# Kernel optimization log

Measured on AMD Instinct MI355X. Metric: run time of the kernel, lower is better.

## Reference

```python
import jax, jax.numpy as jnp
import numpy as np

B, T, C, H, HS = 4, 2048, 1024, 16, 64
EPS = 1e-5


def setup_inputs() -> dict:
    key = jax.random.key(0)
    ks = jax.random.split(key, 16)
    s = lambda k, shp, fan: jax.random.normal(k, shp, jnp.float32) * (fan ** -0.5)
    return {
        "x": jax.random.normal(ks[0], (B, T, C), jnp.float32),
        "wq": s(ks[1], (H, C, HS), C), "bq": jnp.zeros((H, HS), jnp.float32),
        "wk": s(ks[2], (H, C, HS), C), "bk": jnp.zeros((H, HS), jnp.float32),
        "wv": s(ks[3], (H, C, HS), C), "bv": jnp.zeros((H, HS), jnp.float32),
        "wp": s(ks[4], (C, C), C), "bp": jnp.zeros((C,), jnp.float32),
        "w1": s(ks[5], (C, 4 * C), C), "b1": jnp.zeros((4 * C,), jnp.float32),
        "w2": s(ks[6], (4 * C, C), 4 * C), "b2": jnp.zeros((C,), jnp.float32),
        "g1": jnp.ones((C,), jnp.float32), "be1": jnp.zeros((C,), jnp.float32),
        "g2": jnp.ones((C,), jnp.float32), "be2": jnp.zeros((C,), jnp.float32),
    }


def _layernorm(x, g, b):
    mu = jnp.mean(x, axis=-1, keepdims=True)
    var = jnp.mean(jnp.square(x - mu), axis=-1, keepdims=True)
    return (x - mu) * jax.lax.rsqrt(var + EPS) * g + b


def reference(x, wq, bq, wk, bk, wv, bv, wp, bp, w1, b1, w2, b2, g1, be1, g2, be2):
    Bc, Tc, Cc = x.shape
    h = _layernorm(x, g1, be1)
    # per-head projections stacked: [B,H,T,HS]
    q = jnp.einsum('btc,hcd->bhtd', h, wq) + bq[None, :, None, :]
    k = jnp.einsum('btc,hcd->bhtd', h, wk) + bk[None, :, None, :]
    v = jnp.einsum('btc,hcd->bhtd', h, wv) + bv[None, :, None, :]
    # NOTE: source scales by 1/sqrt(n_embd), not 1/sqrt(head_size)
    scores = jnp.einsum('bhtd,bhsd->bhts', q, k) * (Cc ** -0.5)
    causal = jnp.tril(jnp.ones((Tc, Tc), bool))
    scores = jnp.where(causal, scores, -jnp.inf)
    attn = jax.nn.softmax(scores, axis=-1)
    out = jnp.einsum('bhts,bhsd->bhtd', attn, v)
    out = out.transpose(0, 2, 1, 3).reshape(Bc, Tc, Cc)  # concat heads
    x = x + out @ wp + bp
    h2 = _layernorm(x, g2, be2)
    ffn = jax.nn.relu(h2 @ w1 + b1) @ w2 + b2
    return x + ffn
```

## Files before the change

### kernel.cpp

```cpp
#include <hip/hip_runtime.h>


constexpr int Bb = 4, Tt = 2048, Cc = 1024, Hh = 16, HSz = 64, Ff = 4096;
constexpr int Mrows = Bb * Tt;

typedef __attribute__((ext_vector_type(8))) short bf16x8;
typedef __attribute__((ext_vector_type(4))) float f32x4;

__device__ __forceinline__ ushort f2bf(float f) {
  uint u = __builtin_bit_cast(uint, f);
  uint r = (u + 0x7fffu + ((u >> 16) & 1u)) >> 16;
  return (ushort)r;
}
__device__ __forceinline__ float bf2f(ushort s) {
  return __builtin_bit_cast(float, ((uint)s) << 16);
}
__device__ __forceinline__ uint cvtpk_bf16(float lo, float hi) {
  uint r;
  asm("v_cvt_pk_bf16_f32 %0, %1, %2" : "=v"(r) : "v"(lo), "v"(hi));
  return r;
}
__device__ __forceinline__ void gload16(const void* g, void* l) {
  __builtin_amdgcn_global_load_lds(
      (const __attribute__((address_space(1))) void*)g,
      (__attribute__((address_space(3))) void*)l, 16, 0, 0);
}
#define VMCNT0 asm volatile("s_waitcnt vmcnt(0)" ::: "memory")
#define LGKM0                                          \
  do {                                                 \
    asm volatile("s_waitcnt lgkmcnt(0)" ::: "memory"); \
    __builtin_amdgcn_sched_barrier(0);                 \
  } while (0)
#define BARRIER __builtin_amdgcn_s_barrier()

__global__ __launch_bounds__(256) void ln_kernel(const float* __restrict__ x,
                                                 const float* __restrict__ g,
                                                 const float* __restrict__ b,
                                                 ushort* __restrict__ out) {
  int row = blockIdx.x;
  const float* xr = x + (size_t)row * Cc;
  int c4 = threadIdx.x * 4;
  float4 v = *(const float4*)(xr + c4);
  float s1 = v.x + v.y + v.z + v.w;
  float s2 = v.x * v.x + v.y * v.y + v.z * v.z + v.w * v.w;
#pragma unroll
  for (int off = 32; off >= 1; off >>= 1) {
    s1 += __shfl_xor(s1, off);
    s2 += __shfl_xor(s2, off);
  }
  __shared__ float red[8];
  int wid = threadIdx.x >> 6, lane = threadIdx.x & 63;
  if (lane == 0) { red[wid] = s1; red[4 + wid] = s2; }
  __syncthreads();
  float t1 = red[0] + red[1] + red[2] + red[3];
  float t2 = red[4] + red[5] + red[6] + red[7];
  float mu = t1 * (1.0f / Cc);
  float var = t2 * (1.0f / Cc) - mu * mu;
  float rs = rsqrtf(var + 1e-5f);
  float4 gv = *(const float4*)(g + c4);
  float4 bv = *(const float4*)(b + c4);
  ushort4 o;
  o.x = f2bf((v.x - mu) * rs * gv.x + bv.x);
  o.y = f2bf((v.y - mu) * rs * gv.y + bv.y);
  o.z = f2bf((v.z - mu) * rs * gv.z + bv.z);
  o.w = f2bf((v.w - mu) * rs * gv.w + bv.w);
  *(ushort4*)(out + (size_t)row * Cc + c4) = o;
}

__device__ __forceinline__ void tcast_body(const float* __restrict__ src,
                                           ushort* __restrict__ dst, int ldS,
                                           int ldD, int r0, int c0) {
  __shared__ float t[32][33];
  int c = threadIdx.x & 31, r8 = threadIdx.x >> 5;
#pragma unroll
  for (int i = 0; i < 4; ++i) {
    int r = r8 + i * 8;
    t[r][c] = src[(size_t)(r0 + r) * ldS + c0 + c];
  }
  __syncthreads();
#pragma unroll
  for (int i = 0; i < 4; ++i) {
    int rr = r8 + i * 8;
    dst[(size_t)(c0 + rr) * ldD + r0 + c] = f2bf(t[c][rr]);
  }
}

__global__ __launch_bounds__(256) void tcast_kernel(const float* __restrict__ src,
                                                    ushort* __restrict__ dst,
                                                    int ldS, int ldD) {
  tcast_body(src, dst, ldS, ldD, blockIdx.x * 32, blockIdx.y * 32);
}

__global__ __launch_bounds__(256) void tcast_qkv(const float* __restrict__ wq,
                                                 const float* __restrict__ wk,
                                                 const float* __restrict__ wv,
                                                 ushort* __restrict__ dst) {
  int z = blockIdx.z, zz = z >> 4, h = z & 15;
  const float* src = (zz == 0 ? wq : (zz == 1 ? wk : wv)) + (size_t)h * Cc * HSz;
  ushort* d = dst + (size_t)(zz * 1024 + h * 64) * 1024;
  tcast_body(src, d, HSz, Cc, blockIdx.x * 32, blockIdx.y * 32);
}

__global__ __launch_bounds__(256) void bias_concat(const float* __restrict__ bq,
                                                   const float* __restrict__ bk,
                                                   const float* __restrict__ bv,
                                                   float* __restrict__ dst) {
  int i = blockIdx.x * 256 + threadIdx.x;
  dst[i] = i < 1024 ? bq[i] : (i < 2048 ? bk[i - 1024] : bv[i - 2048]);
}

__device__ __forceinline__ void xcd_swz(int& bx, int& by) {
  int bid = blockIdx.x + blockIdx.y * gridDim.x;
  int cpx = (gridDim.x * gridDim.y) >> 3;
  int id = (bid & 7) * cpx + (bid >> 3);
  bx = id % gridDim.x;
  by = id / gridDim.x;
}

template <int MH, int NH>
__device__ __forceinline__ void mfma16(f32x4 (&acc)[8][4], bf16x8 (&a)[4][2],
                                       bf16x8 (&b)[2][2]) {
#pragma unroll
  for (int m = 0; m < 4; ++m)
#pragma unroll
    for (int n = 0; n < 2; ++n)
#pragma unroll
      for (int kk = 0; kk < 2; ++kk)
        acc[MH * 4 + m][NH * 2 + n] = __builtin_amdgcn_mfma_f32_16x16x32_bf16(
            a[m][kk], b[n][kk], acc[MH * 4 + m][NH * 2 + n], 0, 0, 0);
}

__device__ __forceinline__ void gemm256_main(const ushort* __restrict__ A,
                                             const ushort* __restrict__ Bt,
                                             int m0, int n0,
                                             ushort* __restrict__ As,
                                             ushort* __restrict__ Bs,
                                             f32x4 (&acc)[8][4]) {
  constexpr int NKT = 16;
  int tid = threadIdx.x, wid = tid >> 6, lane = tid & 63;
  int wr = wid >> 2, wc = wid & 3, fr = lane & 15, fq = lane >> 4;
  const ushort* Ag = A + (size_t)m0 * 1024;
  const ushort* Bg = Bt + (size_t)n0 * 1024;
  int r0 = tid >> 3, r1 = 64 + (tid >> 3);
  int sc = ((tid & 7) ^ ((tid >> 3) & 7)) << 3;

  auto stage = [&](int ktn, int h, int ns) {
    const ushort* g = (h < 2) ? Ag : Bg;
    ushort* l = ((h < 2) ? As : Bs) + ns * 16384 + (h & 1) * 8192;
    int kcol = ktn * 64, rbase = (h & 1) * 128;
    gload16(g + (size_t)(rbase + r0) * 1024 + kcol + sc, l + (size_t)wid * 512);
    gload16(g + (size_t)(rbase + r1) * 1024 + kcol + sc,
            l + (size_t)(512 + wid * 64) * 8);
  };
  auto readA = [&](int slot, int mh, bf16x8 (&a)[4][2]) {
#pragma unroll
    for (int m = 0; m < 4; ++m) {
      int row = wr * 128 + mh * 64 + m * 16 + fr;
#pragma unroll
      for (int kk = 0; kk < 2; ++kk)
        a[m][kk] = *(const bf16x8*)&As[slot * 16384 + row * 64 +
                                       (((kk * 4 + fq) ^ (row & 7)) << 3)];
    }
  };
  auto readB = [&](int slot, int nh, bf16x8 (&b)[2][2]) {
#pragma unroll
    for (int n = 0; n < 2; ++n) {
      int row = wc * 64 + nh * 32 + n * 16 + fr;
#pragma unroll
      for (int kk = 0; kk < 2; ++kk)
        b[n][kk] = *(const bf16x8*)&Bs[slot * 16384 + row * 64 +
                                       (((kk * 4 + fq) ^ (row & 7)) << 3)];
    }
  };

  stage(0, 0, 0); stage(0, 1, 0); stage(0, 2, 0); stage(0, 3, 0);
  VMCNT0;
  BARRIER;

  bf16x8 a[4][2], b0[2][2], b1[2][2];
#pragma unroll 1
  for (int kt = 0; kt < NKT; ++kt) {
    int slot = kt & 1, ns = slot ^ 1;
    bool st = (kt + 1 < NKT);
    readA(slot, 0, a);
    readB(slot, 0, b0);
    if (st) { stage(kt + 1, 0, ns); stage(kt + 1, 2, ns); }
    BARRIER;
    LGKM0;
    __builtin_amdgcn_s_setprio(1);
    mfma16<0, 0>(acc, a, b0);
    __builtin_amdgcn_s_setprio(0);
    BARRIER;
    readB(slot, 1, b1);
    if (st) { stage(kt + 1, 1, ns); stage(kt + 1, 3, ns); }
    BARRIER;
    LGKM0;
    __builtin_amdgcn_s_setprio(1);
    mfma16<0, 1>(acc, a, b1);
    __builtin_amdgcn_s_setprio(0);
    BARRIER;
    readA(slot, 1, a);
    BARRIER;
    LGKM0;
    __builtin_amdgcn_s_setprio(1);
    mfma16<1, 0>(acc, a, b0);
    __builtin_amdgcn_s_setprio(0);
    BARRIER;
    __builtin_amdgcn_s_setprio(1);
    mfma16<1, 1>(acc, a, b1);
    __builtin_amdgcn_s_setprio(0);
    VMCNT0;
    BARRIER;
  }
}

__global__ __launch_bounds__(512, 2) void gemm256_relu(
    const ushort* __restrict__ A, const ushort* __restrict__ Bt,
    const float* __restrict__ bias, ushort* __restrict__ Cout, int ldc) {
  __shared__ __align__(16) ushort As[2 * 256 * 64];
  __shared__ __align__(16) ushort Bs[2 * 256 * 64];
  f32x4 acc[8][4] = {};
  int bx, by;
  xcd_swz(bx, by);
  int m0 = by * 256, n0 = bx * 256;
  gemm256_main(A, Bt, m0, n0, As, Bs, acc);
  int lane = threadIdx.x & 63, wid = threadIdx.x >> 6;
  int wr = wid >> 2, wc = wid & 3, fr = lane & 15, fq = lane >> 4;
#pragma unroll
  for (int i = 0; i < 8; ++i) {
    int gm = m0 + wr * 128 + (i >> 2) * 64 + (i & 3) * 16 + fq * 4;
#pragma unroll
    for (int j2 = 0; j2 < 4; ++j2) {
      int gn = n0 + wc * 64 + (j2 >> 1) * 32 + (j2 & 1) * 16 + fr;
      float bsv = bias[gn];
#pragma unroll
      for (int j = 0; j < 4; ++j)
        Cout[(size_t)(gm + j) * ldc + gn] = f2bf(fmaxf(acc[i][j2][j] + bsv, 0.f));
    }
  }
}

__global__ __launch_bounds__(512, 2) void gemm256_ffn2(
    const ushort* __restrict__ A, int lda, const ushort* __restrict__ Bt,
    int ldb, const float* __restrict__ bias, const float* __restrict__ res,
    float* __restrict__ Cout, int ldc, int K) {
  __shared__ __align__(16) ushort As[2 * 256 * 64];
  __shared__ __align__(16) ushort Bs[2 * 128 * 64];
  f32x4 acc[8][2] = {};
  int bx, by;
  xcd_swz(bx, by);
  int m0 = by * 256, n0 = bx * 128;
  int tid = threadIdx.x, wid = tid >> 6, lane = tid & 63;
  int wr = wid >> 2, wc = wid & 3, fr = lane & 15, fq = lane >> 4;
  const ushort* Ag = A + (size_t)m0 * lda;
  const ushort* Bg = Bt + (size_t)n0 * ldb;
  int r0 = tid >> 3, r1 = 64 + (tid >> 3);
  int sc = ((tid & 7) ^ ((tid >> 3) & 7)) << 3;
  int NKT = K >> 6;

  auto stageA = [&](int ktn, int h, int ns) {
    ushort* l = As + ns * 16384 + h * 8192;
    int kcol = ktn * 64, rbase = h * 128;
    gload16(Ag + (size_t)(rbase + r0) * lda + kcol + sc, l + (size_t)wid * 512);
    gload16(Ag + (size_t)(rbase + r1) * lda + kcol + sc,
            l + (size_t)(512 + wid * 64) * 8);
  };
  auto stageB = [&](int ktn, int h, int ns) {
    ushort* l = Bs + ns * 8192 + h * 4096;
    int kcol = ktn * 64, rbase = h * 64;
    gload16(Bg + (size_t)(rbase + r0) * ldb + kcol + sc, l + (size_t)wid * 512);
  };
  auto readA = [&](int slot, int mh, bf16x8 (&a)[4][2]) {
#pragma unroll
    for (int m = 0; m < 4; ++m) {
      int row = wr * 128 + mh * 64 + m * 16 + fr;
#pragma unroll
      for (int kk = 0; kk < 2; ++kk)
        a[m][kk] = *(const bf16x8*)&As[slot * 16384 + row * 64 +
                                       (((kk * 4 + fq) ^ (row & 7)) << 3)];
    }
  };
  auto readB = [&](int slot, int nh, bf16x8 (&b)[2]) {
    int row = wc * 32 + nh * 16 + fr;
#pragma unroll
    for (int kk = 0; kk < 2; ++kk)
      b[kk] = *(const bf16x8*)&Bs[slot * 8192 + row * 64 +
                                  (((kk * 4 + fq) ^ (row & 7)) << 3)];
  };
  auto mfma16n = [&](int nh, bf16x8 (&a0)[4][2], bf16x8 (&a1)[4][2],
                     bf16x8 (&b)[2]) {
#pragma unroll
    for (int m = 0; m < 4; ++m)
#pragma unroll
      for (int kk = 0; kk < 2; ++kk)
        acc[m][nh] = __builtin_amdgcn_mfma_f32_16x16x32_bf16(
            a0[m][kk], b[kk], acc[m][nh], 0, 0, 0);
#pragma unroll
    for (int m = 0; m < 4; ++m)
#pragma unroll
      for (int kk = 0; kk < 2; ++kk)
        acc[4 + m][nh] = __builtin_amdgcn_mfma_f32_16x16x32_bf16(
            a1[m][kk], b[kk], acc[4 + m][nh], 0, 0, 0);
  };

  stageA(0, 0, 0); stageA(0, 1, 0); stageB(0, 0, 0); stageB(0, 1, 0);
  VMCNT0;
  BARRIER;

  bf16x8 a0[4][2], a1[4][2], b0[2], b1[2];
#pragma unroll 1
  for (int kt = 0; kt < NKT; ++kt) {
    int slot = kt & 1, ns = slot ^ 1;
    bool st = (kt + 1 < NKT);
    readA(slot, 0, a0);
    readA(slot, 1, a1);
    readB(slot, 0, b0);
    if (st) {
      stageA(kt + 1, 0, ns); stageA(kt + 1, 1, ns);
      stageB(kt + 1, 0, ns); stageB(kt + 1, 1, ns);
    }
    BARRIER;
    LGKM0;
    __builtin_amdgcn_s_setprio(1);
    mfma16n(0, a0, a1, b0);
    __builtin_amdgcn_s_setprio(0);
    BARRIER;
    readB(slot, 1, b1);
    BARRIER;
    LGKM0;
    __builtin_amdgcn_s_setprio(1);
    mfma16n(1, a0, a1, b1);
    __builtin_amdgcn_s_setprio(0);
    VMCNT0;
    BARRIER;
  }

#pragma unroll
  for (int i = 0; i < 8; ++i) {
    int gm = m0 + wr * 128 + (i >> 2) * 64 + (i & 3) * 16 + fq * 4;
#pragma unroll
    for (int nh = 0; nh < 2; ++nh) {
      int gn = n0 + wc * 32 + nh * 16 + fr;
      float bsv = bias[gn];
#pragma unroll
      for (int j = 0; j < 4; ++j) {
        int row = gm + j;
        Cout[(size_t)row * ldc + gn] =
            acc[i][nh][j] + bsv + res[(size_t)row * ldc + gn];
      }
    }
  }
}

__device__ __forceinline__ void gemm_main(const ushort* __restrict__ A, int lda,
                                          const ushort* __restrict__ Bt, int ldb,
                                          int K, int m0, int n0,
                                          ushort* __restrict__ As,
                                          ushort* __restrict__ Bs,
                                          f32x4 (&acc)[4][2]) {
  int tid = threadIdx.x, wid = tid >> 6, lane = tid & 63;
  int wr = wid >> 2, wc = wid & 3, fr = lane & 15, fq = lane >> 4;
  const ushort* Ag = A + (size_t)m0 * lda;
  const ushort* Bg = Bt + (size_t)n0 * ldb;
  for (int k0 = 0; k0 < K; k0 += 64) {
#pragma unroll
    for (int c = 0; c < 2; ++c) {
      int slot = c * 512 + tid;
      int row = slot >> 3, s = slot & 7;
      int sw = (s << 3) ^ ((row & 7) << 3);
      gload16(Ag + (size_t)row * lda + k0 + sw, As + (size_t)(c * 512 + wid * 64) * 8);
      gload16(Bg + (size_t)row * ldb + k0 + sw, Bs + (size_t)(c * 512 + wid * 64) * 8);
    }
    __syncthreads();
    bf16x8 av[4][2], bv[2][2];
#pragma unroll
    for (int m = 0; m < 4; ++m) {
      int row = wr * 64 + m * 16 + fr;
#pragma unroll
      for (int ks = 0; ks < 2; ++ks)
        av[m][ks] = *(const bf16x8*)&As[row * 64 + (((ks * 4 + fq) ^ (row & 7)) << 3)];
    }
#pragma unroll
    for (int n = 0; n < 2; ++n) {
      int row = wc * 32 + n * 16 + fr;
#pragma unroll
      for (int ks = 0; ks < 2; ++ks)
        bv[n][ks] = *(const bf16x8*)&Bs[row * 64 + (((ks * 4 + fq) ^ (row & 7)) << 3)];
    }
#pragma unroll
    for (int m = 0; m < 4; ++m)
#pragma unroll
      for (int n = 0; n < 2; ++n)
#pragma unroll
        for (int ks = 0; ks < 2; ++ks)
          acc[m][n] = __builtin_amdgcn_mfma_f32_16x16x32_bf16(
              av[m][ks], bv[n][ks], acc[m][n], 0, 0, 0);
    __syncthreads();
  }
}

template <bool RELU, bool HASRES, bool OUTBF16>
__global__ __launch_bounds__(512) void gemm_bf16(
    const ushort* __restrict__ A, int lda, const ushort* __restrict__ Bt,
    int ldb, const float* __restrict__ bias, const float* __restrict__ res,
    void* __restrict__ Cout, int ldc, int K) {
  __shared__ __align__(16) ushort As[128 * 64];
  __shared__ __align__(16) ushort Bs[128 * 64];
  f32x4 acc[4][2] = {};
  int bx, by;
  xcd_swz(bx, by);
  int m0 = by * 128, n0 = bx * 128;
  gemm_main(A, lda, Bt, ldb, K, m0, n0, As, Bs, acc);
  int lane = threadIdx.x & 63, wid = threadIdx.x >> 6;
  int wr = wid >> 2, wc = wid & 3, fr = lane & 15, fq = lane >> 4;
#pragma unroll
  for (int m = 0; m < 4; ++m) {
    int gm = m0 + wr * 64 + m * 16 + fq * 4;
#pragma unroll
    for (int n = 0; n < 2; ++n) {
      int gn = n0 + wc * 32 + n * 16 + fr;
      float bsv = bias[gn];
#pragma unroll
      for (int j = 0; j < 4; ++j) {
        int row = gm + j;
        float v = acc[m][n][j] + bsv;
        if constexpr (HASRES) v += res[(size_t)row * ldc + gn];
        if constexpr (RELU) v = fmaxf(v, 0.f);
        if constexpr (OUTBF16)
          ((ushort*)Cout)[(size_t)row * ldc + gn] = f2bf(v);
        else
          ((float*)Cout)[(size_t)row * ldc + gn] = v;
      }
    }
  }
}

__global__ __launch_bounds__(512) void gemm_qkv(const ushort* __restrict__ A,
                                                const ushort* __restrict__ Bt,
                                                const float* __restrict__ bias,
                                                ushort* __restrict__ q,
                                                ushort* __restrict__ k,
                                                ushort* __restrict__ vt) {
  __shared__ __align__(16) ushort As[128 * 64];
  __shared__ __align__(16) ushort Bs[128 * 64];
  f32x4 acc[4][2] = {};
  int bx, by;
  xcd_swz(bx, by);
  int m0 = by * 128, n0 = bx * 128;
  gemm_main(A, 1024, Bt, 1024, 1024, m0, n0, As, Bs, acc);
  int lane = threadIdx.x & 63, wid = threadIdx.x >> 6;
  int wr = wid >> 2, wc = wid & 3, fr = lane & 15, fq = lane >> 4;
  const float qscale = 1.4426950408889634f / 32.0f;
#pragma unroll
  for (int m = 0; m < 4; ++m) {
    int gm = m0 + wr * 64 + m * 16 + fq * 4;
#pragma unroll
    for (int n = 0; n < 2; ++n) {
      int gn = n0 + wc * 32 + n * 16 + fr;
      float bsv = bias[gn];
      if (gn < 1024) {
#pragma unroll
        for (int j = 0; j < 4; ++j)
          q[(size_t)(gm + j) * 1024 + gn] = f2bf((acc[m][n][j] + bsv) * qscale);
      } else if (gn < 2048) {
        int col = gn - 1024;
#pragma unroll
        for (int j = 0; j < 4; ++j)
          k[(size_t)(gm + j) * 1024 + col] = f2bf(acc[m][n][j] + bsv);
      } else {
        int dd = gn - 2048, h = dd >> 6, d = dd & 63;
        int bbr = gm >> 11, t = gm & 2047;
        ushort4 pw = {f2bf(acc[m][n][0] + bsv), f2bf(acc[m][n][1] + bsv),
                      f2bf(acc[m][n][2] + bsv), f2bf(acc[m][n][3] + bsv)};
        *(ushort4*)&vt[(((size_t)(bbr * 16 + h)) * 64 + d) * 2048 + t] = pw;
      }
    }
  }
}

constexpr int QB = 128, KVB = 64;
__global__ __launch_bounds__(512) void attn_kernel(const ushort* __restrict__ Qb,
                                                   const ushort* __restrict__ Kb,
                                                   const ushort* __restrict__ Vt,
                                                   ushort* __restrict__ att) {
  __shared__ __align__(16) ushort Klds[2][64 * 64];
  __shared__ __align__(16) ushort Vlds[2][64 * 64];
  __shared__ __align__(16) ushort Plds[8][16 * 64];
  int tid = threadIdx.x, wid = tid >> 6, lane = tid & 63;
  int fr = lane & 15, fq = lane >> 4;
  int bh = blockIdx.y, bb = bh >> 4, hh = bh & 15;
  const ushort* qkbase = Qb + ((size_t)bb * Tt) * Cc + hh * HSz;
  const ushort* Kbase = Kb + ((size_t)bb * Tt) * Cc + hh * HSz;
  const ushort* Vbase = Vt + ((size_t)(bb * Hh + hh)) * HSz * Tt;
  int srow = tid >> 3;
  int ssw = ((tid & 7) << 3) ^ ((srow & 7) << 3);

#pragma unroll 1
  for (int pass = 0; pass < 2; ++pass) {
    int qt = pass ? (Tt / QB - 1 - (int)blockIdx.x) : (int)blockIdx.x;
    int q0 = qt * QB;
    int q0w = q0 + wid * 16;

    bf16x8 Qreg[2];
#pragma unroll
    for (int d2 = 0; d2 < 2; ++d2)
      Qreg[d2] = *(const bf16x8*)(qkbase + (size_t)(q0w + fr) * Cc + d2 * 32 + fq * 8);
    f32x4 Oa[4] = {};
    float mrow = -1e30f, lrow = 0.f;
    int nt = q0 / KVB + 2;

    __syncthreads();
    gload16(Kbase + (size_t)srow * Cc + ssw, (char*)Klds[0] + wid * 1024);
    gload16(Vbase + (size_t)srow * Tt + ssw, (char*)Vlds[0] + wid * 1024);

#pragma unroll 1
    for (int kt = 0; kt < nt; ++kt) {
      int t0 = kt * KVB;
      int c = kt & 1;
      __syncthreads();
      if (kt + 1 < nt) {
        int t0n = t0 + KVB;
        gload16(Kbase + (size_t)(t0n + srow) * Cc + ssw,
                (char*)Klds[c ^ 1] + wid * 1024);
        gload16(Vbase + (size_t)srow * Tt + t0n + ssw,
                (char*)Vlds[c ^ 1] + wid * 1024);
      }
      if (q0w + 15 < t0) continue;

      const char* Kc = (const char*)Klds[c];
      const char* Vc = (const char*)Vlds[c];
      bf16x8 kf[4][2];
#pragma unroll
      for (int ks = 0; ks < 4; ++ks)
#pragma unroll
        for (int d2 = 0; d2 < 2; ++d2) {
          int row = ks * 16 + fr;
          int off = (d2 * 64 + fq * 16) ^ ((row & 7) << 4);
          kf[ks][d2] = *(const bf16x8*)(Kc + row * 128 + off);
        }
      f32x4 accs[4] = {};
      __builtin_amdgcn_s_setprio(1);
#pragma unroll
      for (int ks = 0; ks < 4; ++ks) {
        accs[ks] = __builtin_amdgcn_mfma_f32_16x16x32_bf16(
            kf[ks][0], Qreg[0], accs[ks], 0, 0, 0);
        accs[ks] = __builtin_amdgcn_mfma_f32_16x16x32_bf16(
            kf[ks][1], Qreg[1], accs[ks], 0, 0, 0);
      }
      __builtin_amdgcn_s_setprio(0);

      float sv[4][4];
      float vmax = -1e30f;
      if (t0 + 63 <= q0w) {
#pragma unroll
        for (int ks = 0; ks < 4; ++ks)
#pragma unroll
          for (int j = 0; j < 4; ++j) {
            sv[ks][j] = accs[ks][j];
            vmax = fmaxf(vmax, sv[ks][j]);
          }
      } else {
        int qg = q0w + fr;
#pragma unroll
        for (int ks = 0; ks < 4; ++ks)
#pragma unroll
          for (int j = 0; j < 4; ++j) {
            int kg = t0 + ks * 16 + fq * 4 + j;
            float s = accs[ks][j];
            s = (kg <= qg) ? s : -1e30f;
            sv[ks][j] = s;
            vmax = fmaxf(vmax, s);
          }
      }
      float mnew = mrow;
      if (!__all(vmax <= mrow + 11.0f)) {
        float rmax = fmaxf(vmax, __shfl_xor(vmax, 16));
        rmax = fmaxf(rmax, __shfl_xor(rmax, 32));
        mnew = fmaxf(mrow, rmax);
        float sf = exp2f(mrow - mnew);
        mrow = mnew;
        lrow *= sf;
#pragma unroll
        for (int j = 0; j < 4; ++j) {
          float sfo = __shfl(sf, fq * 4 + j);
#pragma unroll
          for (int ds = 0; ds < 4; ++ds) Oa[ds][j] *= sfo;
        }
      }
      char* pbase = (char*)Plds[wid] + fr * 128;
#pragma unroll
      for (int ks = 0; ks < 4; ++ks) {
        float p0 = exp2f(sv[ks][0] - mnew);
        float p1 = exp2f(sv[ks][1] - mnew);
        float p2 = exp2f(sv[ks][2] - mnew);
        float p3 = exp2f(sv[ks][3] - mnew);
        lrow += (p0 + p1) + (p2 + p3);
        uint2 pw = {cvtpk_bf16(p0, p1), cvtpk_bf16(p2, p3)};
        int off = (ks * 32 + fq * 8) ^ ((fr & 7) << 4);
        *(uint2*)(pbase + off) = pw;
      }

      bf16x8 vf[4][2];
#pragma unroll
      for (int ds = 0; ds < 4; ++ds)
#pragma unroll
        for (int k2 = 0; k2 < 2; ++k2) {
          int row = ds * 16 + fr;
          int off = (k2 * 64 + fq * 16) ^ ((row & 7) << 4);
          vf[ds][k2] = *(const bf16x8*)(Vc + row * 128 + off);
        }
      bf16x8 pf[2];
#pragma unroll
      for (int k2 = 0; k2 < 2; ++k2) {
        int off = (k2 * 64 + fq * 16) ^ ((fr & 7) << 4);
        pf[k2] = *(const bf16x8*)((const char*)Plds[wid] + fr * 128 + off);
      }
      __builtin_amdgcn_s_setprio(1);
#pragma unroll
      for (int ds = 0; ds < 4; ++ds) {
        Oa[ds] = __builtin_amdgcn_mfma_f32_16x16x32_bf16(
            pf[0], vf[ds][0], Oa[ds], 0, 0, 0);
        Oa[ds] = __builtin_amdgcn_mfma_f32_16x16x32_bf16(
            pf[1], vf[ds][1], Oa[ds], 0, 0, 0);
      }
      __builtin_amdgcn_s_setprio(0);
    }

    {
      lrow += __shfl_xor(lrow, 16);
      lrow += __shfl_xor(lrow, 32);
      float linv = 1.f / lrow;
#pragma unroll
      for (int j = 0; j < 4; ++j) {
        float lo = __shfl(linv, fq * 4 + j);
        int qg = q0w + fq * 4 + j;
        ushort* orow = att + (size_t)(bb * Tt + qg) * Cc + hh * HSz;
#pragma unroll
        for (int ds = 0; ds < 4; ++ds)
          orow[ds * 16 + fr] = f2bf(Oa[ds][j] * lo);
      }
    }
  }
}

extern "C" void kernel_launch(void* const* d_in, const int* in_sizes, int n_in,
                              void* d_out, int out_size, void* d_ws,
                              size_t ws_size, hipStream_t stream) {
  const float* x = (const float*)d_in[0];
  const float* wq = (const float*)d_in[1];
  const float* bq = (const float*)d_in[2];
  const float* wk = (const float*)d_in[3];
  const float* bk = (const float*)d_in[4];
  const float* wv = (const float*)d_in[5];
  const float* bv = (const float*)d_in[6];
  const float* wp = (const float*)d_in[7];
  const float* bp = (const float*)d_in[8];
  const float* w1 = (const float*)d_in[9];
  const float* b1 = (const float*)d_in[10];
  const float* w2 = (const float*)d_in[11];
  const float* b2 = (const float*)d_in[12];
  const float* g1 = (const float*)d_in[13];
  const float* be1 = (const float*)d_in[14];
  const float* g2 = (const float*)d_in[15];
  const float* be2 = (const float*)d_in[16];
  float* out = (float*)d_out;

  ushort* Qb = (ushort*)d_ws;
  ushort* Kb = Qb + (size_t)8388608;
  ushort* Vt = Kb + (size_t)8388608;
  ushort* att = Vt + (size_t)8388608;
  ushort* ffh = Qb;
  ushort* h1b = att + (size_t)8388608;
  float* x2 = (float*)(h1b + (size_t)8388608);
  ushort* wqkvT = (ushort*)(x2 + (size_t)8388608);
  ushort* wpT = wqkvT + (size_t)3145728;
  ushort* w1T = wpT + (size_t)1048576;
  ushort* w2T = w1T + (size_t)4194304;
  float* bqkv = (float*)(w2T + (size_t)4194304);

  tcast_qkv<<<dim3(32, 2, 48), 256, 0, stream>>>(wq, wk, wv, wqkvT);
  tcast_kernel<<<dim3(32, 32), 256, 0, stream>>>(wp, wpT, 1024, 1024);
  tcast_kernel<<<dim3(32, 128), 256, 0, stream>>>(w1, w1T, 4096, 1024);
  tcast_kernel<<<dim3(128, 32), 256, 0, stream>>>(w2, w2T, 1024, 4096);
  bias_concat<<<dim3(12), 256, 0, stream>>>(bq, bk, bv, bqkv);

  ln_kernel<<<dim3(Mrows), 256, 0, stream>>>(x, g1, be1, h1b);
  gemm_qkv<<<dim3(24, 64), 512, 0, stream>>>(h1b, wqkvT, bqkv, Qb, Kb, Vt);
  attn_kernel<<<dim3(Tt / QB / 2, Bb * Hh), 512, 0, stream>>>(Qb, Kb, Vt, att);
  gemm_bf16<false, true, false><<<dim3(8, 64), 512, 0, stream>>>(
      att, 1024, wpT, 1024, bp, x, x2, 1024, 1024);
  ln_kernel<<<dim3(Mrows), 256, 0, stream>>>(x2, g2, be2, h1b);
  gemm256_relu<<<dim3(16, 32), 512, 0, stream>>>(h1b, w1T, b1, ffh, 4096);
  gemm256_ffn2<<<dim3(8, 32), 512, 0, stream>>>(
      ffh, 4096, w2T, 4096, b2, x2, out, 1024, 4096);
}
```

Measured before the change: 359.2 us.

## Triple-buffer FFN2 GEMM loads with counted vmcnt waits

The FFN down-projection GEMM moves from double to triple buffering in LDS: it issues global-to-LDS loads two K-tiles ahead and waits only for the current tile with a partial vmcnt count instead of draining all loads. The per-iteration body is also flattened into one read phase and one MFMA phase, which drops several intermediate barriers. The goal is to hide more global memory latency and cut synchronisation. The cost is a larger LDS footprint per block and reliance on exact per-tile load counts for the vmcnt values.

```diff
diff --git a/kernel.cpp b/kernel.cpp
--- a/kernel.cpp
+++ b/kernel.cpp
@@ -25,7 +25,7 @@
       (const __attribute__((address_space(1))) void*)g,
       (__attribute__((address_space(3))) void*)l, 16, 0, 0);
 }
-#define VMCNT0 asm volatile("s_waitcnt vmcnt(0)" ::: "memory")
+#define VMCNT(n) asm volatile("s_waitcnt vmcnt(" #n ")" ::: "memory")
 #define LGKM0                                          \
   do {                                                 \
     asm volatile("s_waitcnt lgkmcnt(0)" ::: "memory"); \
@@ -174,7 +174,7 @@
   };
 
   stage(0, 0, 0); stage(0, 1, 0); stage(0, 2, 0); stage(0, 3, 0);
-  VMCNT0;
+  VMCNT(0);
   BARRIER;
 
   bf16x8 a[4][2], b0[2][2], b1[2][2];
@@ -209,7 +209,7 @@
     __builtin_amdgcn_s_setprio(1);
     mfma16<1, 1>(acc, a, b1);
     __builtin_amdgcn_s_setprio(0);
-    VMCNT0;
+    VMCNT(0);
     BARRIER;
   }
 }
@@ -244,8 +244,8 @@
     const ushort* __restrict__ A, int lda, const ushort* __restrict__ Bt,
     int ldb, const float* __restrict__ bias, const float* __restrict__ res,
     float* __restrict__ Cout, int ldc, int K) {
-  __shared__ __align__(16) ushort As[2 * 256 * 64];
-  __shared__ __align__(16) ushort Bs[2 * 128 * 64];
+  __shared__ __align__(16) ushort As[3 * 256 * 64];
+  __shared__ __align__(16) ushort Bs[3 * 128 * 64];
   f32x4 acc[8][2] = {};
   int bx, by;
   xcd_swz(bx, by);
@@ -287,51 +287,58 @@
       b[kk] = *(const bf16x8*)&Bs[slot * 8192 + row * 64 +
                                   (((kk * 4 + fq) ^ (row & 7)) << 3)];
   };
-  auto mfma16n = [&](int nh, bf16x8 (&a0)[4][2], bf16x8 (&a1)[4][2],
-                     bf16x8 (&b)[2]) {
-#pragma unroll
-    for (int m = 0; m < 4; ++m)
-#pragma unroll
-      for (int kk = 0; kk < 2; ++kk)
-        acc[m][nh] = __builtin_amdgcn_mfma_f32_16x16x32_bf16(
-            a0[m][kk], b[kk], acc[m][nh], 0, 0, 0);
-#pragma unroll
-    for (int m = 0; m < 4; ++m)
-#pragma unroll
-      for (int kk = 0; kk < 2; ++kk)
-        acc[4 + m][nh] = __builtin_amdgcn_mfma_f32_16x16x32_bf16(
-            a1[m][kk], b[kk], acc[4 + m][nh], 0, 0, 0);
+  auto stageTile = [&](int ktn, int ns) {
+    stageA(ktn, 0, ns); stageA(ktn, 1, ns);
+    stageB(ktn, 0, ns); stageB(ktn, 1, ns);
   };
 
-  stageA(0, 0, 0); stageA(0, 1, 0); stageB(0, 0, 0); stageB(0, 1, 0);
-  VMCNT0;
-  BARRIER;
+  stageTile(0, 0);
+  if (NKT > 1) stageTile(1, 1);
 
   bf16x8 a0[4][2], a1[4][2], b0[2], b1[2];
 #pragma unroll 1
   for (int kt = 0; kt < NKT; ++kt) {
-    int slot = kt & 1, ns = slot ^ 1;
-    bool st = (kt + 1 < NKT);
+    int slot = kt % 3;
+    if (kt + 2 < NKT) {
+      stageTile(kt + 2, (kt + 2) % 3);
+      VMCNT(12);
+    } else if (kt + 1 < NKT) {
+      VMCNT(6);
+    } else {
+      VMCNT(0);
+    }
+    BARRIER;
     readA(slot, 0, a0);
     readA(slot, 1, a1);
     readB(slot, 0, b0);
-    if (st) {
-      stageA(kt + 1, 0, ns); stageA(kt + 1, 1, ns);
-      stageB(kt + 1, 0, ns); stageB(kt + 1, 1, ns);
-    }
-    BARRIER;
+    readB(slot, 1, b1);
     LGKM0;
     __builtin_amdgcn_s_setprio(1);
-    mfma16n(0, a0, a1, b0);
+#pragma unroll
+    for (int m = 0; m < 4; ++m)
+#pragma unroll
+      for (int kk = 0; kk < 2; ++kk)
+        acc[m][0] = __builtin_amdgcn_mfma_f32_16x16x32_bf16(
+            a0[m][kk], b0[kk], acc[m][0], 0, 0, 0);
+#pragma unroll
+    for (int m = 0; m < 4; ++m)
+#pragma unroll
+      for (int kk = 0; kk < 2; ++kk)
+        acc[4 + m][0] = __builtin_amdgcn_mfma_f32_16x16x32_bf16(
+            a1[m][kk], b0[kk], acc[4 + m][0], 0, 0, 0);
+#pragma unroll
+    for (int m = 0; m < 4; ++m)
+#pragma unroll
+      for (int kk = 0; kk < 2; ++kk)
+        acc[m][1] = __builtin_amdgcn_mfma_f32_16x16x32_bf16(
+            a0[m][kk], b1[kk], acc[m][1], 0, 0, 0);
+#pragma unroll
+    for (int m = 0; m < 4; ++m)
+#pragma unroll
+      for (int kk = 0; kk < 2; ++kk)
+        acc[4 + m][1] = __builtin_amdgcn_mfma_f32_16x16x32_bf16(
+            a1[m][kk], b1[kk], acc[4 + m][1], 0, 0, 0);
     __builtin_amdgcn_s_setprio(0);
-    BARRIER;
-    readB(slot, 1, b1);
-    BARRIER;
-    LGKM0;
-    __builtin_amdgcn_s_setprio(1);
-    mfma16n(1, a0, a1, b1);
-    __builtin_amdgcn_s_setprio(0);
-    VMCNT0;
     BARRIER;
   }
 
```

Result: slower. 370.5 us (+3.1%).

## Use 256x192 tiled QKV GEMM and route FFN2 through generic 128-tile GEMM

Applied to the files above, without the earlier changes.

Replaces the 128x128-tile QKV projection with a new 256x192-tile double-buffered kernel that splits the next tile's loads across three MFMA phases, giving 16x32=512 blocks. This raises arithmetic intensity per block and reduces the number of small tiles. The dedicated 256x128 FFN2 kernel is removed and FFN2 now runs on the generic gemm_bf16 path with 128x128 tiles. That path may reuse less data per block on the K=4096 GEMM.

```diff
diff --git a/kernel.cpp b/kernel.cpp
--- a/kernel.cpp
+++ b/kernel.cpp
@@ -25,7 +25,7 @@
       (const __attribute__((address_space(1))) void*)g,
       (__attribute__((address_space(3))) void*)l, 16, 0, 0);
 }
-#define VMCNT0 asm volatile("s_waitcnt vmcnt(0)" ::: "memory")
+#define VMCNT(n) asm volatile("s_waitcnt vmcnt(" #n ")" ::: "memory")
 #define LGKM0                                          \
   do {                                                 \
     asm volatile("s_waitcnt lgkmcnt(0)" ::: "memory"); \
@@ -174,7 +174,7 @@
   };
 
   stage(0, 0, 0); stage(0, 1, 0); stage(0, 2, 0); stage(0, 3, 0);
-  VMCNT0;
+  VMCNT(0);
   BARRIER;
 
   bf16x8 a[4][2], b0[2][2], b1[2][2];
@@ -209,7 +209,7 @@
     __builtin_amdgcn_s_setprio(1);
     mfma16<1, 1>(acc, a, b1);
     __builtin_amdgcn_s_setprio(0);
-    VMCNT0;
+    VMCNT(0);
     BARRIER;
   }
 }
@@ -240,35 +240,33 @@
   }
 }
 
-__global__ __launch_bounds__(512, 2) void gemm256_ffn2(
-    const ushort* __restrict__ A, int lda, const ushort* __restrict__ Bt,
-    int ldb, const float* __restrict__ bias, const float* __restrict__ res,
-    float* __restrict__ Cout, int ldc, int K) {
+__global__ __launch_bounds__(512, 2) void gemm192_qkv(
+    const ushort* __restrict__ A, const ushort* __restrict__ Bt,
+    const float* __restrict__ bias, ushort* __restrict__ q,
+    ushort* __restrict__ k, ushort* __restrict__ vt) {
   __shared__ __align__(16) ushort As[2 * 256 * 64];
-  __shared__ __align__(16) ushort Bs[2 * 128 * 64];
-  f32x4 acc[8][2] = {};
+  __shared__ __align__(16) ushort Bs[2 * 192 * 64];
+  f32x4 acc[8][3] = {};
   int bx, by;
   xcd_swz(bx, by);
-  int m0 = by * 256, n0 = bx * 128;
+  int m0 = by * 256, n0 = bx * 192;
   int tid = threadIdx.x, wid = tid >> 6, lane = tid & 63;
   int wr = wid >> 2, wc = wid & 3, fr = lane & 15, fq = lane >> 4;
-  const ushort* Ag = A + (size_t)m0 * lda;
-  const ushort* Bg = Bt + (size_t)n0 * ldb;
-  int r0 = tid >> 3, r1 = 64 + (tid >> 3);
+  const ushort* Ag = A + (size_t)m0 * 1024;
+  const ushort* Bg = Bt + (size_t)n0 * 1024;
+  int r0 = tid >> 3;
   int sc = ((tid & 7) ^ ((tid >> 3) & 7)) << 3;
-  int NKT = K >> 6;
-
-  auto stageA = [&](int ktn, int h, int ns) {
-    ushort* l = As + ns * 16384 + h * 8192;
-    int kcol = ktn * 64, rbase = h * 128;
-    gload16(Ag + (size_t)(rbase + r0) * lda + kcol + sc, l + (size_t)wid * 512);
-    gload16(Ag + (size_t)(rbase + r1) * lda + kcol + sc,
-            l + (size_t)(512 + wid * 64) * 8);
-  };
-  auto stageB = [&](int ktn, int h, int ns) {
-    ushort* l = Bs + ns * 8192 + h * 4096;
-    int kcol = ktn * 64, rbase = h * 64;
-    gload16(Bg + (size_t)(rbase + r0) * ldb + kcol + sc, l + (size_t)wid * 512);
+  constexpr int NKT = 16;
+
+  auto stageA = [&](int ktn, int c, int ns) {
+    ushort* l = As + ns * 16384 + c * 4096;
+    gload16(Ag + (size_t)(c * 64 + r0) * 1024 + ktn * 64 + sc,
+            l + (size_t)wid * 512);
+  };
+  auto stageB = [&](int ktn, int c, int ns) {
+    ushort* l = Bs + ns * 12288 + c * 4096;
+    gload16(Bg + (size_t)(c * 64 + r0) * 1024 + ktn * 64 + sc,
+            l + (size_t)wid * 512);
   };
   auto readA = [&](int slot, int mh, bf16x8 (&a)[4][2]) {
 #pragma unroll
@@ -281,10 +279,10 @@
     }
   };
   auto readB = [&](int slot, int nh, bf16x8 (&b)[2]) {
-    int row = wc * 32 + nh * 16 + fr;
+    int row = wc * 48 + nh * 16 + fr;
 #pragma unroll
     for (int kk = 0; kk < 2; ++kk)
-      b[kk] = *(const bf16x8*)&Bs[slot * 8192 + row * 64 +
+      b[kk] = *(const bf16x8*)&Bs[slot * 12288 + row * 64 +
                                   (((kk * 4 + fq) ^ (row & 7)) << 3)];
   };
   auto mfma16n = [&](int nh, bf16x8 (&a0)[4][2], bf16x8 (&a1)[4][2],
@@ -303,11 +301,12 @@
             a1[m][kk], b[kk], acc[4 + m][nh], 0, 0, 0);
   };
 
-  stageA(0, 0, 0); stageA(0, 1, 0); stageB(0, 0, 0); stageB(0, 1, 0);
-  VMCNT0;
+  stageA(0, 0, 0); stageA(0, 1, 0); stageA(0, 2, 0); stageA(0, 3, 0);
+  stageB(0, 0, 0); stageB(0, 1, 0); stageB(0, 2, 0);
+  VMCNT(0);
   BARRIER;
 
-  bf16x8 a0[4][2], a1[4][2], b0[2], b1[2];
+  bf16x8 a0[4][2], a1[4][2], b0[2], b1[2], b2[2];
 #pragma unroll 1
   for (int kt = 0; kt < NKT; ++kt) {
     int slot = kt & 1, ns = slot ^ 1;
@@ -315,10 +314,7 @@
     readA(slot, 0, a0);
     readA(slot, 1, a1);
     readB(slot, 0, b0);
-    if (st) {
-      stageA(kt + 1, 0, ns); stageA(kt + 1, 1, ns);
-      stageB(kt + 1, 0, ns); stageB(kt + 1, 1, ns);
-    }
+    if (st) { stageA(kt + 1, 0, ns); stageA(kt + 1, 1, ns); stageB(kt + 1, 0, ns); }
     BARRIER;
     LGKM0;
     __builtin_amdgcn_s_setprio(1);
@@ -326,27 +322,47 @@
     __builtin_amdgcn_s_setprio(0);
     BARRIER;
     readB(slot, 1, b1);
+    if (st) { stageA(kt + 1, 2, ns); stageA(kt + 1, 3, ns); stageB(kt + 1, 1, ns); }
     BARRIER;
     LGKM0;
     __builtin_amdgcn_s_setprio(1);
     mfma16n(1, a0, a1, b1);
     __builtin_amdgcn_s_setprio(0);
-    VMCNT0;
-    BARRIER;
-  }
-
+    BARRIER;
+    readB(slot, 2, b2);
+    if (st) { stageB(kt + 1, 2, ns); }
+    BARRIER;
+    LGKM0;
+    __builtin_amdgcn_s_setprio(1);
+    mfma16n(2, a0, a1, b2);
+    __builtin_amdgcn_s_setprio(0);
+    VMCNT(0);
+    BARRIER;
+  }
+
+  const float qscale = 1.4426950408889634f / 32.0f;
 #pragma unroll
   for (int i = 0; i < 8; ++i) {
     int gm = m0 + wr * 128 + (i >> 2) * 64 + (i & 3) * 16 + fq * 4;
 #pragma unroll
-    for (int nh = 0; nh < 2; ++nh) {
-      int gn = n0 + wc * 32 + nh * 16 + fr;
+    for (int nh = 0; nh < 3; ++nh) {
+      int gn = n0 + wc * 48 + nh * 16 + fr;
       float bsv = bias[gn];
-#pragma unroll
-      for (int j = 0; j < 4; ++j) {
-        int row = gm + j;
-        Cout[(size_t)row * ldc + gn] =
-            acc[i][nh][j] + bsv + res[(size_t)row * ldc + gn];
+      if (gn < 1024) {
+#pragma unroll
+        for (int j = 0; j < 4; ++j)
+          q[(size_t)(gm + j) * 1024 + gn] = f2bf((acc[i][nh][j] + bsv) * qscale);
+      } else if (gn < 2048) {
+        int col = gn - 1024;
+#pragma unroll
+        for (int j = 0; j < 4; ++j)
+          k[(size_t)(gm + j) * 1024 + col] = f2bf(acc[i][nh][j] + bsv);
+      } else {
+        int dd = gn - 2048, h = dd >> 6, d = dd & 63;
+        int bbr = gm >> 11, t = gm & 2047;
+        ushort4 pw = {f2bf(acc[i][nh][0] + bsv), f2bf(acc[i][nh][1] + bsv),
+                      f2bf(acc[i][nh][2] + bsv), f2bf(acc[i][nh][3] + bsv)};
+        *(ushort4*)&vt[(((size_t)(bbr * 16 + h)) * 64 + d) * 2048 + t] = pw;
       }
     }
   }
@@ -430,49 +446,6 @@
           ((ushort*)Cout)[(size_t)row * ldc + gn] = f2bf(v);
         else
           ((float*)Cout)[(size_t)row * ldc + gn] = v;
-      }
-    }
-  }
-}
-
-__global__ __launch_bounds__(512) void gemm_qkv(const ushort* __restrict__ A,
-                                                const ushort* __restrict__ Bt,
-                                                const float* __restrict__ bias,
-                                                ushort* __restrict__ q,
-                                                ushort* __restrict__ k,
-                                                ushort* __restrict__ vt) {
-  __shared__ __align__(16) ushort As[128 * 64];
-  __shared__ __align__(16) ushort Bs[128 * 64];
-  f32x4 acc[4][2] = {};
-  int bx, by;
-  xcd_swz(bx, by);
-  int m0 = by * 128, n0 = bx * 128;
-  gemm_main(A, 1024, Bt, 1024, 1024, m0, n0, As, Bs, acc);
-  int lane = threadIdx.x & 63, wid = threadIdx.x >> 6;
-  int wr = wid >> 2, wc = wid & 3, fr = lane & 15, fq = lane >> 4;
-  const float qscale = 1.4426950408889634f / 32.0f;
-#pragma unroll
-  for (int m = 0; m < 4; ++m) {
-    int gm = m0 + wr * 64 + m * 16 + fq * 4;
-#pragma unroll
-    for (int n = 0; n < 2; ++n) {
-      int gn = n0 + wc * 32 + n * 16 + fr;
-      float bsv = bias[gn];
-      if (gn < 1024) {
-#pragma unroll
-        for (int j = 0; j < 4; ++j)
-          q[(size_t)(gm + j) * 1024 + gn] = f2bf((acc[m][n][j] + bsv) * qscale);
-      } else if (gn < 2048) {
-        int col = gn - 1024;
-#pragma unroll
-        for (int j = 0; j < 4; ++j)
-          k[(size_t)(gm + j) * 1024 + col] = f2bf(acc[m][n][j] + bsv);
-      } else {
-        int dd = gn - 2048, h = dd >> 6, d = dd & 63;
-        int bbr = gm >> 11, t = gm & 2047;
-        ushort4 pw = {f2bf(acc[m][n][0] + bsv), f2bf(acc[m][n][1] + bsv),
-                      f2bf(acc[m][n][2] + bsv), f2bf(acc[m][n][3] + bsv)};
-        *(ushort4*)&vt[(((size_t)(bbr * 16 + h)) * 64 + d) * 2048 + t] = pw;
       }
     }
   }
@@ -685,12 +658,12 @@
   bias_concat<<<dim3(12), 256, 0, stream>>>(bq, bk, bv, bqkv);
 
   ln_kernel<<<dim3(Mrows), 256, 0, stream>>>(x, g1, be1, h1b);
-  gemm_qkv<<<dim3(24, 64), 512, 0, stream>>>(h1b, wqkvT, bqkv, Qb, Kb, Vt);
+  gemm192_qkv<<<dim3(16, 32), 512, 0, stream>>>(h1b, wqkvT, bqkv, Qb, Kb, Vt);
   attn_kernel<<<dim3(Tt / QB / 2, Bb * Hh), 512, 0, stream>>>(Qb, Kb, Vt, att);
   gemm_bf16<false, true, false><<<dim3(8, 64), 512, 0, stream>>>(
       att, 1024, wpT, 1024, bp, x, x2, 1024, 1024);
   ln_kernel<<<dim3(Mrows), 256, 0, stream>>>(x2, g2, be2, h1b);
   gemm256_relu<<<dim3(16, 32), 512, 0, stream>>>(h1b, w1T, b1, ffh, 4096);
-  gemm256_ffn2<<<dim3(8, 32), 512, 0, stream>>>(
+  gemm_bf16<false, true, false><<<dim3(8, 64), 512, 0, stream>>>(
       ffh, 4096, w2T, 4096, b2, x2, out, 1024, 4096);
 }
```

New measurement: 350.7 us. 1.02x faster.
